# Performance work log

Measured on AMD Instinct MI355X. Metric: run time of the kernel, lower is better.

## Reference

```python
import jax, jax.numpy as jnp
import numpy as np

SEQ_FEAT = 1024   # sequence_length (input feature dim of Linear layers)
ATT = 512         # attention_size
P_DROP = 0.2
B, T = 8, 2048


def setup_inputs() -> dict:
    key = jax.random.key(0)
    k1, k2, k3, k4, k5 = jax.random.split(key, 5)
    s = 1.0 / np.sqrt(SEQ_FEAT)
    x = jax.random.normal(k1, (B, T, SEQ_FEAT), dtype=jnp.float32)
    Wq = jax.random.normal(k2, (ATT, SEQ_FEAT), dtype=jnp.float32) * s
    Wk = jax.random.normal(k3, (ATT, SEQ_FEAT), dtype=jnp.float32) * s
    Wv = jax.random.normal(k4, (SEQ_FEAT, SEQ_FEAT), dtype=jnp.float32) * s
    drop_mask = jax.random.uniform(k5, (B, T, T)) >= P_DROP  # keep where True
    return {"x": x, "Wq": Wq, "Wk": Wk, "Wv": Wv, "drop_mask": drop_mask}


def reference(x, Wq, Wk, Wv, drop_mask):
    # Linear (no bias): y = x @ W.T, torch Linear weight is [out, in]
    q = jnp.einsum('btf,af->bta', x, Wq)          # [B,T,ATT]
    k = jnp.einsum('btf,af->bta', x, Wk)          # [B,T,ATT]
    v = jnp.einsum('btf,gf->btg', x, Wv)          # [B,T,SEQ_FEAT]
    scores = jnp.einsum('bta,bsa->bts', q, k) / jnp.sqrt(jnp.float32(ATT))
    attn = jax.nn.softmax(scores, axis=-1)
    # dropout (training=True in F.dropout): scale kept entries by 1/(1-p)
    attn = jnp.where(drop_mask, attn / (1.0 - P_DROP), 0.0)
    out = jnp.einsum('bts,bsg->btg', attn, v)     # [B,T,SEQ_FEAT]
    return out
```

## Files before the change

kernel.cpp:

```cpp
#include <hip/hip_runtime.h>

typedef unsigned short u16;
typedef _Float16 h16;
typedef __attribute__((ext_vector_type(4))) float f32x4;
typedef __attribute__((ext_vector_type(8))) _Float16 h16x8;
typedef __attribute__((ext_vector_type(4))) _Float16 h16x4;
typedef __attribute__((ext_vector_type(4))) int i32x4;

__global__ __launch_bounds__(256) void k_cast_all(
    const float* __restrict__ x, const float* __restrict__ wq,
    const float* __restrict__ wk, const float* __restrict__ wv,
    h16* __restrict__ xf, h16* __restrict__ wqk, h16* __restrict__ wvf) {
  int bid = blockIdx.x;
  const float* src;
  h16* dst;
  int idx;
  if (bid < 16384) { src = x;  dst = xf;           idx = bid * 256 + threadIdx.x; }
  else if (bid < 16896) { src = wq; dst = wqk;          idx = (bid - 16384) * 256 + threadIdx.x; }
  else if (bid < 17408) { src = wk; dst = wqk + 524288; idx = (bid - 16896) * 256 + threadIdx.x; }
  else { src = wv; dst = wvf;          idx = (bid - 17408) * 256 + threadIdx.x; }
  f32x4 v = ((const f32x4*)src)[idx];
  h16x4 o;
#pragma unroll
  for (int e = 0; e < 4; ++e) o[e] = (h16)v[e];
  ((h16x4*)dst)[idx] = o;
}

__device__ __forceinline__ void gl16(const u16* src, u16* dst) {
  __builtin_amdgcn_global_load_lds(
      (const __attribute__((address_space(1))) unsigned*)src,
      (__attribute__((address_space(3))) unsigned*)dst, 16, 0, 0);
}

__device__ __forceinline__ void swz_block(int& bn, int& bm, int& bz) {
  int gx = gridDim.x, gy = gridDim.y;
  int flat = blockIdx.x + gx * (blockIdx.y + gy * blockIdx.z);
  int nwg = gx * gy * (int)gridDim.z;
  int q = nwg >> 3;
  int id = (flat & 7) * q + (flat >> 3);
  bn = id % gx;
  id /= gx;
  bm = id % gy;
  bz = id / gy;
}

template <int NT, int EPI>
__global__ __launch_bounds__(512, 2) void k_gemm(
    const u16* __restrict__ A, int lda, long long aZ,
    const u16* __restrict__ B, int ldb, long long bZ,
    void* __restrict__ Cp, int ldc, long long cZ, float scale) {
  __shared__ u16 lds[2 * 32768];
  int bn, bm, bz;
  swz_block(bn, bm, bz);
  const int tid = threadIdx.x;
  const int lane = tid & 63, wid = tid >> 6;
  const int wr = wid >> 2, wc = wid & 3;
  const u16* A0 = A + (size_t)bz * aZ + (size_t)bm * 256 * lda;
  const u16* B0 = B + (size_t)bz * bZ + (size_t)bn * 256 * ldb;

  const int lc = ((tid & 3) ^ ((tid >> 3) & 3)) << 3;
  const int r0s = tid >> 2;

  auto STAGE = [&](int t, int op, int kh) {
    if (t >= NT) return;
    int kk = (t << 6) + (kh << 5);
    const u16* g = op ? B0 : A0;
    int ld_ = op ? ldb : lda;
    u16* dst = &lds[0] + (t & 1) * 32768 + op * 16384 + kh * 8192;
    gl16(g + (size_t)r0s * ld_ + kk + lc, dst + tid * 8);
    gl16(g + (size_t)(r0s + 128) * ld_ + kk + lc, dst + 4096 + tid * 8);
  };

  const int fr = lane & 15;
  const int pch = (((lane >> 4) ^ ((fr >> 1) & 3)) << 3);
  const int abase = (wr * 128 + fr) * 32 + pch;
  const int bbase = 16384 + (wc * 64 + fr) * 32 + pch;

  f32x4 acc[8][4] = {};

  STAGE(0, 0, 0); STAGE(0, 0, 1); STAGE(0, 1, 0); STAGE(0, 1, 1);
  asm volatile("s_waitcnt vmcnt(0)" ::: "memory");
  __builtin_amdgcn_s_barrier();
  asm volatile("" ::: "memory");

#pragma unroll 1
  for (int T = 0; T < NT; ++T) {
    const int cb = (T & 1) * 32768;
    h16x8 av[8], bv[4];
#pragma unroll
    for (int n = 0; n < 4; ++n) bv[n] = *(const h16x8*)&lds[cb + bbase + n * 512];
#pragma unroll
    for (int m = 0; m < 8; ++m) av[m] = *(const h16x8*)&lds[cb + abase + m * 512];
    STAGE(T + 1, 0, 0); STAGE(T + 1, 0, 1); STAGE(T + 1, 1, 0); STAGE(T + 1, 1, 1);
    __builtin_amdgcn_s_setprio(1);
#pragma unroll
    for (int m = 0; m < 8; ++m)
#pragma unroll
      for (int n = 0; n < 4; ++n)
        acc[m][n] = __builtin_amdgcn_mfma_f32_16x16x32_f16(av[m], bv[n], acc[m][n], 0, 0, 0);
    __builtin_amdgcn_s_setprio(0);
#pragma unroll
    for (int n = 0; n < 4; ++n) bv[n] = *(const h16x8*)&lds[cb + bbase + 8192 + n * 512];
#pragma unroll
    for (int m = 0; m < 8; ++m) av[m] = *(const h16x8*)&lds[cb + abase + 8192 + m * 512];
    __builtin_amdgcn_s_setprio(1);
#pragma unroll
    for (int m = 0; m < 8; ++m)
#pragma unroll
      for (int n = 0; n < 4; ++n)
        acc[m][n] = __builtin_amdgcn_mfma_f32_16x16x32_f16(av[m], bv[n], acc[m][n], 0, 0, 0);
    __builtin_amdgcn_s_setprio(0);
    asm volatile("s_waitcnt vmcnt(0)" ::: "memory");
    __builtin_amdgcn_s_barrier();
    asm volatile("" ::: "memory");
  }

  const size_t zc = (size_t)bz * cZ;
#pragma unroll
  for (int m = 0; m < 8; ++m)
#pragma unroll
    for (int n = 0; n < 4; ++n)
#pragma unroll
      for (int r = 0; r < 4; ++r) {
        int row = bm * 256 + wr * 128 + m * 16 + (lane >> 4) * 4 + r;
        int col = bn * 256 + wc * 64 + n * 16 + fr;
        float f = acc[m][n][r];
        if constexpr (EPI == 0) {
          ((h16*)Cp)[zc + (size_t)row * ldc + col] = (h16)f;
        } else if constexpr (EPI == 1) {
          ((float*)Cp)[zc + (size_t)row * ldc + col] = f * scale;
        } else {
          ((h16*)Cp)[zc + (size_t)row * ldc + col] = (h16)(f * scale);
        }
      }
}

__global__ __launch_bounds__(256) void k_softmax(const h16* __restrict__ sc,
                                                 h16* __restrict__ P,
                                                 const int* __restrict__ mask) {
  const size_t rowp = blockIdx.x;
  const h16* srow = sc + rowp * 2048;
  h16* prow = P + rowp * 2048;
  const int* mrow = mask + rowp * 2048;
  const int tid = threadIdx.x;
  h16x8 hv = ((const h16x8*)srow)[tid];
  float v[8];
#pragma unroll
  for (int j = 0; j < 8; ++j) v[j] = (float)hv[j];
  float m = v[0];
#pragma unroll
  for (int j = 1; j < 8; ++j) m = fmaxf(m, v[j]);
#pragma unroll
  for (int o = 32; o >= 1; o >>= 1) m = fmaxf(m, __shfl_xor(m, o));
  __shared__ float redm[4], reds[4];
  if ((tid & 63) == 0) redm[tid >> 6] = m;
  __syncthreads();
  m = fmaxf(fmaxf(redm[0], redm[1]), fmaxf(redm[2], redm[3]));
  float e[8], s = 0.f;
#pragma unroll
  for (int j = 0; j < 8; ++j) { e[j] = __expf(v[j] - m); s += e[j]; }
#pragma unroll
  for (int o = 32; o >= 1; o >>= 1) s += __shfl_xor(s, o);
  if ((tid & 63) == 0) reds[tid >> 6] = s;
  __syncthreads();
  s = reds[0] + reds[1] + reds[2] + reds[3];
  const float inv = 1.0f / (0.8f * s);
  i32x4 m0 = ((const i32x4*)mrow)[tid * 2];
  i32x4 m1 = ((const i32x4*)mrow)[tid * 2 + 1];
  int mm[8] = {m0[0], m0[1], m0[2], m0[3], m1[0], m1[1], m1[2], m1[3]};
  h16x8 o;
#pragma unroll
  for (int j = 0; j < 8; ++j) o[j] = mm[j] ? (h16)(e[j] * inv) : (h16)0.f;
  ((h16x8*)prow)[tid] = o;
}

extern "C" void kernel_launch(void* const* d_in, const int* in_sizes, int n_in,
                              void* d_out, int out_size, void* d_ws, size_t ws_size,
                              hipStream_t stream) {
  const float* x  = (const float*)d_in[0];
  const float* Wq = (const float*)d_in[1];
  const float* Wk = (const float*)d_in[2];
  const float* Wv = (const float*)d_in[3];
  const int* mask = (const int*)d_in[4];
  float* out = (float*)d_out;

  u16* ws = (u16*)d_ws;
  h16* xf  = (h16*)ws;
  h16* Wqk = (h16*)(ws + 16777216);
  h16* Wvf = (h16*)(ws + 17825792);
  h16* qk  = (h16*)(ws + 18874368);
  h16* vvt = (h16*)(ws + 35651584);
  h16* Pb  = (h16*)(ws + 52428864);
  h16* sch = (h16*)(ws + 85983296);

  k_cast_all<<<18432, 256, 0, stream>>>(x, Wq, Wk, Wv, xf, Wqk, Wvf);

  dim3 gqk(4, 64, 1);
  k_gemm<16, 0><<<gqk, 512, 0, stream>>>((const u16*)xf, 1024, 0,
                                         (const u16*)Wqk, 1024, 0, qk, 1024, 0, 0.f);

  dim3 gvt(64, 4, 1);
  k_gemm<16, 0><<<gvt, 512, 0, stream>>>((const u16*)Wvf, 1024, 0,
                                         (const u16*)xf, 1024, 0, vvt, 16384, 0, 0.f);

  const float scale = 0.044194173824159216f;
  dim3 gs(8, 8, 8);
  k_gemm<8, 4><<<gs, 512, 0, stream>>>((const u16*)qk, 1024, 2097152,
                                       (const u16*)(qk + 512), 1024, 2097152,
                                       sch, 2048, 4194304, scale);

  k_softmax<<<16384, 256, 0, stream>>>(sch, Pb, mask);

  dim3 gpv(4, 8, 8);
  k_gemm<32, 1><<<gpv, 512, 0, stream>>>((const u16*)Pb, 2048, 4194304,
                                         (const u16*)vvt, 16384, 2048,
                                         out, 1024, 2097152, 1.0f);

  (void)in_sizes; (void)n_in; (void)out_size; (void)ws_size;
}
```

Before: 272.3 us.

## Switch GEMM to triple-buffered K=32 stages with two-deep prefetch

The GEMM main loop drops the double-buffered K=64 tile (two K=32 halves) in favour of a three-slot ring of K=32 tiles. Loads run two iterations ahead and each barrier waits with vmcnt(4) instead of draining all outstanding loads, so global-to-LDS traffic overlaps MFMA work better. LDS use falls from 128 KB to 96 KB per block. In exchange there are twice as many loop iterations and barriers per GEMM, and the template NT values are doubled to match.

```diff
diff --git a/kernel.cpp b/kernel.cpp
--- a/kernel.cpp
+++ b/kernel.cpp
@@ -49,49 +49,51 @@
     const u16* __restrict__ A, int lda, long long aZ,
     const u16* __restrict__ B, int ldb, long long bZ,
     void* __restrict__ Cp, int ldc, long long cZ, float scale) {
-  __shared__ u16 lds[2 * 32768];
+  __shared__ u16 lds[3 * 16384];
   int bn, bm, bz;
   swz_block(bn, bm, bz);
   const int tid = threadIdx.x;
-  const int lane = tid & 63, wid = tid >> 6;
-  const int wr = wid >> 2, wc = wid & 3;
+  const int lane = tid & 63;
+  const int wr = (tid >> 6) >> 2, wc = (tid >> 6) & 3;
   const u16* A0 = A + (size_t)bz * aZ + (size_t)bm * 256 * lda;
   const u16* B0 = B + (size_t)bz * bZ + (size_t)bn * 256 * ldb;
 
   const int lc = ((tid & 3) ^ ((tid >> 3) & 3)) << 3;
   const int r0s = tid >> 2;
 
-  auto STAGE = [&](int t, int op, int kh) {
+  auto STAGE = [&](int t, int slot) {
     if (t >= NT) return;
-    int kk = (t << 6) + (kh << 5);
-    const u16* g = op ? B0 : A0;
-    int ld_ = op ? ldb : lda;
-    u16* dst = &lds[0] + (t & 1) * 32768 + op * 16384 + kh * 8192;
-    gl16(g + (size_t)r0s * ld_ + kk + lc, dst + tid * 8);
-    gl16(g + (size_t)(r0s + 128) * ld_ + kk + lc, dst + 4096 + tid * 8);
+    int kk = t << 5;
+    u16* dst = &lds[0] + slot * 16384;
+    gl16(A0 + (size_t)r0s * lda + kk + lc, dst + tid * 8);
+    gl16(A0 + (size_t)(r0s + 128) * lda + kk + lc, dst + 4096 + tid * 8);
+    gl16(B0 + (size_t)r0s * ldb + kk + lc, dst + 8192 + tid * 8);
+    gl16(B0 + (size_t)(r0s + 128) * ldb + kk + lc, dst + 12288 + tid * 8);
   };
 
   const int fr = lane & 15;
   const int pch = (((lane >> 4) ^ ((fr >> 1) & 3)) << 3);
   const int abase = (wr * 128 + fr) * 32 + pch;
-  const int bbase = 16384 + (wc * 64 + fr) * 32 + pch;
+  const int bbase = 8192 + (wc * 64 + fr) * 32 + pch;
 
   f32x4 acc[8][4] = {};
 
-  STAGE(0, 0, 0); STAGE(0, 0, 1); STAGE(0, 1, 0); STAGE(0, 1, 1);
-  asm volatile("s_waitcnt vmcnt(0)" ::: "memory");
+  STAGE(0, 0);
+  STAGE(1, 1);
+  asm volatile("s_waitcnt vmcnt(4)" ::: "memory");
   __builtin_amdgcn_s_barrier();
   asm volatile("" ::: "memory");
 
+  int slot = 0, pslot = 2;
 #pragma unroll 1
   for (int T = 0; T < NT; ++T) {
-    const int cb = (T & 1) * 32768;
+    const int sb = slot * 16384;
     h16x8 av[8], bv[4];
 #pragma unroll
-    for (int n = 0; n < 4; ++n) bv[n] = *(const h16x8*)&lds[cb + bbase + n * 512];
-#pragma unroll
-    for (int m = 0; m < 8; ++m) av[m] = *(const h16x8*)&lds[cb + abase + m * 512];
-    STAGE(T + 1, 0, 0); STAGE(T + 1, 0, 1); STAGE(T + 1, 1, 0); STAGE(T + 1, 1, 1);
+    for (int n = 0; n < 4; ++n) bv[n] = *(const h16x8*)&lds[sb + bbase + n * 512];
+#pragma unroll
+    for (int m = 0; m < 8; ++m) av[m] = *(const h16x8*)&lds[sb + abase + m * 512];
+    STAGE(T + 2, pslot);
     __builtin_amdgcn_s_setprio(1);
 #pragma unroll
     for (int m = 0; m < 8; ++m)
@@ -99,20 +101,14 @@
       for (int n = 0; n < 4; ++n)
         acc[m][n] = __builtin_amdgcn_mfma_f32_16x16x32_f16(av[m], bv[n], acc[m][n], 0, 0, 0);
     __builtin_amdgcn_s_setprio(0);
-#pragma unroll
-    for (int n = 0; n < 4; ++n) bv[n] = *(const h16x8*)&lds[cb + bbase + 8192 + n * 512];
-#pragma unroll
-    for (int m = 0; m < 8; ++m) av[m] = *(const h16x8*)&lds[cb + abase + 8192 + m * 512];
-    __builtin_amdgcn_s_setprio(1);
-#pragma unroll
-    for (int m = 0; m < 8; ++m)
-#pragma unroll
-      for (int n = 0; n < 4; ++n)
-        acc[m][n] = __builtin_amdgcn_mfma_f32_16x16x32_f16(av[m], bv[n], acc[m][n], 0, 0, 0);
-    __builtin_amdgcn_s_setprio(0);
-    asm volatile("s_waitcnt vmcnt(0)" ::: "memory");
+    if (T < NT - 2)
+      asm volatile("s_waitcnt vmcnt(4)" ::: "memory");
+    else
+      asm volatile("s_waitcnt vmcnt(0)" ::: "memory");
     __builtin_amdgcn_s_barrier();
     asm volatile("" ::: "memory");
+    slot = (slot == 2) ? 0 : slot + 1;
+    pslot = (pslot == 2) ? 0 : pslot + 1;
   }
 
   const size_t zc = (size_t)bz * cZ;
@@ -196,23 +192,23 @@
   k_cast_all<<<18432, 256, 0, stream>>>(x, Wq, Wk, Wv, xf, Wqk, Wvf);
 
   dim3 gqk(4, 64, 1);
-  k_gemm<16, 0><<<gqk, 512, 0, stream>>>((const u16*)xf, 1024, 0,
+  k_gemm<32, 0><<<gqk, 512, 0, stream>>>((const u16*)xf, 1024, 0,
                                          (const u16*)Wqk, 1024, 0, qk, 1024, 0, 0.f);
 
   dim3 gvt(64, 4, 1);
-  k_gemm<16, 0><<<gvt, 512, 0, stream>>>((const u16*)Wvf, 1024, 0,
+  k_gemm<32, 0><<<gvt, 512, 0, stream>>>((const u16*)Wvf, 1024, 0,
                                          (const u16*)xf, 1024, 0, vvt, 16384, 0, 0.f);
 
   const float scale = 0.044194173824159216f;
   dim3 gs(8, 8, 8);
-  k_gemm<8, 4><<<gs, 512, 0, stream>>>((const u16*)qk, 1024, 2097152,
-                                       (const u16*)(qk + 512), 1024, 2097152,
-                                       sch, 2048, 4194304, scale);
+  k_gemm<16, 4><<<gs, 512, 0, stream>>>((const u16*)qk, 1024, 2097152,
+                                        (const u16*)(qk + 512), 1024, 2097152,
+                                        sch, 2048, 4194304, scale);
 
   k_softmax<<<16384, 256, 0, stream>>>(sch, Pb, mask);
 
   dim3 gpv(4, 8, 8);
-  k_gemm<32, 1><<<gpv, 512, 0, stream>>>((const u16*)Pb, 2048, 4194304,
+  k_gemm<64, 1><<<gpv, 512, 0, stream>>>((const u16*)Pb, 2048, 4194304,
                                          (const u16*)vvt, 16384, 2048,
                                          out, 1024, 2097152, 1.0f);
 
```

After: 269.3 us. Within noise of the previous version (-1.1%).
